# Performance work log

Measured on AMD Instinct MI355X. Metric: run time of the kernel, lower is better.

Reference implementation:

```python
import jax, jax.numpy as jnp
import numpy as np

N = 65536      # total nodes
E = 655360     # total edges
G = 256        # graphs in batch
EGO = 64       # ego ids per graph (max(ego)+1)
S = G * EGO    # global ego segments
C_IN, H, P, OUT, L = 128, 128, 64, 10, 3
EPS = 1e-5


def setup_inputs() -> dict:
    key = jax.random.key(0)
    ks = jax.random.split(key, 8)
    x = jax.random.normal(ks[0], (N, C_IN), dtype=jnp.float32)
    edge_index = jax.random.randint(ks[1], (2, E), 0, N)
    batch = jnp.repeat(jnp.arange(G), N // G)          # sorted graph ids
    ego = jnp.arange(N) % EGO                           # every ego segment non-empty
    s = 1.0 / np.sqrt(H)
    w_root = jax.random.normal(ks[2], (L, H, H), jnp.float32) * s
    w_rel = jax.random.normal(ks[3], (L, H, H), jnp.float32) * s
    b_conv = jnp.zeros((L, H), jnp.float32)
    down_w = jax.random.normal(ks[4], (H, P), jnp.float32) * s
    w1 = jax.random.normal(ks[5], (P, 2 * OUT), jnp.float32) * (1.0 / np.sqrt(P))
    b1 = jnp.zeros((2 * OUT,), jnp.float32)
    gamma = jnp.ones((2 * OUT,), jnp.float32)
    beta = jnp.zeros((2 * OUT,), jnp.float32)
    w2 = jax.random.normal(ks[6], (2 * OUT, OUT), jnp.float32) * (1.0 / np.sqrt(2 * OUT))
    b2 = jnp.zeros((OUT,), jnp.float32)
    return dict(x=x, edge_index=edge_index, batch=batch, ego=ego,
                w_root=w_root, w_rel=w_rel, b_conv=b_conv, down_w=down_w,
                w1=w1, b1=b1, gamma=gamma, beta=beta, w2=w2, b2=b2)


def reference(x, edge_index, batch, ego, w_root, w_rel, b_conv, down_w,
              w1, b1, gamma, beta, w2, b2):
    src, dst = edge_index[0], edge_index[1]
    h = x
    for l in range(L):  # GraphConv: lin_rel(sum_{j->i} h_j) + lin_root(h_i) + b, then ReLU
        agg = jax.ops.segment_sum(h[src], dst, num_segments=N)      # [N,H]
        h = jax.nn.relu(agg @ w_rel[l] + h @ w_root[l] + b_conv[l])
    xi = h @ down_w                                                  # [N,P]
    ego_g = ego + batch * EGO                                        # global ego id
    pooled = jax.ops.segment_sum(xi, ego_g, num_segments=S)          # global_add_pool -> [S,P]
    seg_batch = jax.ops.segment_max(batch, ego_g, num_segments=S)    # global_max_pool(batch, ego) -> [S]
    # SoftmaxAggregation(t=1): per-feature softmax over ego segments within each graph
    m = jax.ops.segment_max(pooled, seg_batch, num_segments=G)       # [G,P]
    e = jnp.exp(pooled - m[seg_batch])
    denom = jax.ops.segment_sum(e, seg_batch, num_segments=G)
    alpha = jax.lax.stop_gradient(e / denom[seg_batch])              # semi_grad=True
    g = jax.ops.segment_sum(alpha * pooled, seg_batch, num_segments=G)  # [G,P]
    # PyG MLP([P, 2*OUT, OUT]): Linear -> BatchNorm (batch stats) -> ReLU -> Linear
    z = g @ w1 + b1
    mu = z.mean(axis=0)
    var = z.var(axis=0)
    z = (z - mu) / jnp.sqrt(var + EPS) * gamma + beta
    z = jax.nn.relu(z)
    return z @ w2 + b2                                               # [G,OUT]
```

## Files before the change

kernel.cpp:

```cpp
#include <hip/hip_runtime.h>
#include <hip/hip_bf16.h>

#define NN 65536
#define EE 655360
#define GG 256
#define EGOC 64
#define SS (GG*EGOC)
#define HH 128
#define PP 64
#define OUTD 10
#define LLAYERS 3
#define PADW 40
#define EPB1 5120
#define BCAP 4096

typedef __attribute__((ext_vector_type(8))) short short8_t;
typedef __attribute__((ext_vector_type(4))) float f32x4_t;

__device__ __forceinline__ unsigned short f2bf(float f){
  unsigned u = __float_as_uint(f);
  unsigned r = (u + 0x7fffu + ((u >> 16) & 1u)) >> 16;
  return (unsigned short)r;
}
__device__ __forceinline__ float bflo(unsigned v){ return __uint_as_float(v << 16); }
__device__ __forceinline__ float bfhi(unsigned v){ return __uint_as_float(v & 0xffff0000u); }

__global__ __launch_bounds__(256) void prep(const float* __restrict__ x,
    unsigned short* __restrict__ xb, int* __restrict__ bcur,
    const float* __restrict__ w_rel, const float* __restrict__ w_root,
    unsigned short* __restrict__ wt){
  const int b = blockIdx.x;
  if (b < 4096){
    if (b == 0) bcur[threadIdx.x] = 0;
    const size_t i = ((size_t)b * 256 + threadIdx.x) * 8;
    float4 a = *(const float4*)(x + i);
    float4 v = *(const float4*)(x + i + 4);
    uint4 o;
    o.x = f2bf(a.x) | ((unsigned)f2bf(a.y) << 16);
    o.y = f2bf(a.z) | ((unsigned)f2bf(a.w) << 16);
    o.z = f2bf(v.x) | ((unsigned)f2bf(v.y) << 16);
    o.w = f2bf(v.z) | ((unsigned)f2bf(v.w) << 16);
    *(uint4*)(xb + i) = o;
  } else {
    const int idx = (b - 4096) * 256 + threadIdx.x;
    const int mi = idx >> 14;
    const int n = (idx >> 7) & 127, k = idx & 127;
    const float* src = (mi & 1) ? w_root : w_rel;
    const int l = mi >> 1;
    wt[idx] = f2bf(src[(size_t)l * 16384 + (size_t)k * 128 + n]);
  }
}

__global__ __launch_bounds__(256) void bucket1(const int* __restrict__ src,
    const int* __restrict__ dst, int* __restrict__ bucket_cursor,
    unsigned* __restrict__ bdata){
  __shared__ int hist[256], lbase[256], cur[256], rbase[256];
  __shared__ unsigned staged[EPB1];
  const int t = threadIdx.x;
  const int e0 = blockIdx.x * EPB1;
  hist[t] = 0;
  __syncthreads();
  #pragma unroll
  for (int k = 0; k < EPB1/256; ++k){
    int d = dst[e0 + t + k*256];
    atomicAdd(&hist[d >> 8], 1);
  }
  __syncthreads();
  const int cnt = hist[t];
  int val = cnt;
  for (int off = 1; off < 256; off <<= 1){
    int y = (t >= off) ? hist[t - off] : 0;
    __syncthreads();
    val += y;
    hist[t] = val;
    __syncthreads();
  }
  const int excl = val - cnt;
  lbase[t] = excl;
  cur[t] = excl;
  rbase[t] = atomicAdd(&bucket_cursor[t], cnt);
  __syncthreads();
  #pragma unroll
  for (int k = 0; k < EPB1/256; ++k){
    int i = e0 + t + k*256;
    int d = dst[i];
    int s = src[i];
    int b = d >> 8;
    int p = atomicAdd(&cur[b], 1);
    staged[p] = (unsigned)s | ((unsigned)(d & 255) << 16) | ((unsigned)b << 24);
  }
  __syncthreads();
  #pragma unroll
  for (int k = 0; k < EPB1/256; ++k){
    int i = t + k*256;
    unsigned w = staged[i];
    int b = w >> 24;
    bdata[b * BCAP + rbase[b] + (i - lbase[b])] = w;
  }
}

__global__ __launch_bounds__(256) void bucket2(const unsigned* __restrict__ bdata,
    const int* __restrict__ bucket_cursor, int* __restrict__ rowptr,
    int* __restrict__ csr){
  __shared__ int hist[256], cur[256], red[256];
  const int t = threadIdx.x;
  const int b = blockIdx.x;
  red[t] = (t < b) ? bucket_cursor[t] : 0;
  hist[t] = 0;
  __syncthreads();
  for (int off = 128; off > 0; off >>= 1){
    if (t < off) red[t] += red[t + off];
    __syncthreads();
  }
  const int base = red[0];
  const int cnt = bucket_cursor[b];
  const unsigned* bd = bdata + (size_t)b * BCAP;
  for (int i = t; i < cnt; i += 256)
    atomicAdd(&hist[(bd[i] >> 16) & 255], 1);
  __syncthreads();
  const int c = hist[t];
  int val = c;
  for (int off = 1; off < 256; off <<= 1){
    int y = (t >= off) ? hist[t - off] : 0;
    __syncthreads();
    val += y;
    hist[t] = val;
    __syncthreads();
  }
  const int excl = val - c;
  cur[t] = excl;
  rowptr[(b << 8) + t] = base + excl;
  if (b == 255 && t == 255) rowptr[NN] = EE;
  __syncthreads();
  for (int i = t; i < cnt; i += 256){
    unsigned w = bd[i];
    int dl = (w >> 16) & 255;
    int p = atomicAdd(&cur[dl], 1);
    csr[base + p] = (int)(w & 0xFFFFu);
  }
}

__global__ __launch_bounds__(256) void agg_bf(const unsigned* __restrict__ hb,
    const int* __restrict__ rowptr, const int* __restrict__ csr,
    unsigned* __restrict__ aggb){
  const int wid = threadIdx.x >> 6;
  const int lane = threadIdx.x & 63;
  const int sub = lane >> 4;
  const int c = lane & 15;
  int node = (blockIdx.x << 2) + wid;

  int beg = rowptr[node];
  int end = rowptr[node + 1];
  int sw0, sw1, sw2, sw3;
  {
    int e0 = beg + sub, e1 = beg + 4 + sub, e2 = beg + 8 + sub, e3 = beg + 12 + sub;
    sw0 = csr[e0 < end ? e0 : beg];
    sw1 = csr[e1 < end ? e1 : beg];
    sw2 = csr[e2 < end ? e2 : beg];
    sw3 = csr[e3 < end ? e3 : beg];
  }

  for (int g = 0; g < 8; ++g){
    uint4 w0 = *(const uint4*)(hb + ((size_t)sw0 << 6) + (c << 2));
    uint4 w1 = *(const uint4*)(hb + ((size_t)sw1 << 6) + (c << 2));
    uint4 w2 = *(const uint4*)(hb + ((size_t)sw2 << 6) + (c << 2));
    uint4 w3 = *(const uint4*)(hb + ((size_t)sw3 << 6) + (c << 2));
    int nbeg = 0, nend = 0;
    if (g < 7){
      nbeg = rowptr[node + 8192];
      nend = rowptr[node + 8193];
    }
    float a0=0.f,a1=0.f,a2=0.f,a3=0.f,a4=0.f,a5=0.f,a6=0.f,a7=0.f;
    if (beg + sub      < end){ a0+=bflo(w0.x); a1+=bfhi(w0.x); a2+=bflo(w0.y); a3+=bfhi(w0.y);
                               a4+=bflo(w0.z); a5+=bfhi(w0.z); a6+=bflo(w0.w); a7+=bfhi(w0.w); }
    if (beg + 4 + sub  < end){ a0+=bflo(w1.x); a1+=bfhi(w1.x); a2+=bflo(w1.y); a3+=bfhi(w1.y);
                               a4+=bflo(w1.z); a5+=bfhi(w1.z); a6+=bflo(w1.w); a7+=bfhi(w1.w); }
    if (beg + 8 + sub  < end){ a0+=bflo(w2.x); a1+=bfhi(w2.x); a2+=bflo(w2.y); a3+=bfhi(w2.y);
                               a4+=bflo(w2.z); a5+=bfhi(w2.z); a6+=bflo(w2.w); a7+=bfhi(w2.w); }
    if (beg + 12 + sub < end){ a0+=bflo(w3.x); a1+=bfhi(w3.x); a2+=bflo(w3.y); a3+=bfhi(w3.y);
                               a4+=bflo(w3.z); a5+=bfhi(w3.z); a6+=bflo(w3.w); a7+=bfhi(w3.w); }
    for (int j = beg + 16; j < end; j += 16){
      #pragma unroll
      for (int u = 0; u < 4; ++u){
        const int e = j + (u << 2) + sub;
        if (e < end){
          const int s = csr[e];
          uint4 w = *(const uint4*)(hb + ((size_t)s << 6) + (c << 2));
          a0 += bflo(w.x); a1 += bfhi(w.x);
          a2 += bflo(w.y); a3 += bfhi(w.y);
          a4 += bflo(w.z); a5 += bfhi(w.z);
          a6 += bflo(w.w); a7 += bfhi(w.w);
        }
      }
    }
    a0 += __shfl_xor(a0, 16, 64); a1 += __shfl_xor(a1, 16, 64);
    a2 += __shfl_xor(a2, 16, 64); a3 += __shfl_xor(a3, 16, 64);
    a4 += __shfl_xor(a4, 16, 64); a5 += __shfl_xor(a5, 16, 64);
    a6 += __shfl_xor(a6, 16, 64); a7 += __shfl_xor(a7, 16, 64);
    a0 += __shfl_xor(a0, 32, 64); a1 += __shfl_xor(a1, 32, 64);
    a2 += __shfl_xor(a2, 32, 64); a3 += __shfl_xor(a3, 32, 64);
    a4 += __shfl_xor(a4, 32, 64); a5 += __shfl_xor(a5, 32, 64);
    a6 += __shfl_xor(a6, 32, 64); a7 += __shfl_xor(a7, 32, 64);
    if (lane < 16){
      uint4 o;
      o.x = (unsigned)f2bf(a0) | ((unsigned)f2bf(a1) << 16);
      o.y = (unsigned)f2bf(a2) | ((unsigned)f2bf(a3) << 16);
      o.z = (unsigned)f2bf(a4) | ((unsigned)f2bf(a5) << 16);
      o.w = (unsigned)f2bf(a6) | ((unsigned)f2bf(a7) << 16);
      *(uint4*)(aggb + ((size_t)node << 6) + (c << 2)) = o;
    }
    if (g < 7){
      node += 8192;
      beg = nbeg; end = nend;
      int e0 = beg + sub, e1 = beg + 4 + sub, e2 = beg + 8 + sub, e3 = beg + 12 + sub;
      sw0 = csr[e0 < end ? e0 : beg];
      sw1 = csr[e1 < end ? e1 : beg];
      sw2 = csr[e2 < end ? e2 : beg];
      sw3 = csr[e3 < end ? e3 : beg];
    }
  }
}

__global__ __launch_bounds__(256) void conv_mfma(
    const unsigned short* __restrict__ Aagg, const unsigned short* __restrict__ Ah,
    const unsigned short* __restrict__ wt,
    const float* __restrict__ bias,
    unsigned short* __restrict__ out){
  __shared__ unsigned short As[2][128 * PADW];
  __shared__ unsigned short Ws[2][128 * PADW];
  const int tid = threadIdx.x;
  const int row0 = blockIdx.x << 7;
  const int lane = tid & 63, wid = tid >> 6;
  const int wm64 = (wid >> 1) << 6;
  const int wn64 = (wid & 1) << 6;
  const int fr = lane & 15;
  const int fs = (lane >> 4) << 3;
  const int r0 = tid >> 2;
  const int s8 = (tid & 3) << 3;

  f32x4_t acc[4][4];
  #pragma unroll
  for (int i = 0; i < 4; ++i)
    #pragma unroll
    for (int j = 0; j < 4; ++j) acc[i][j] = (f32x4_t){0.f,0.f,0.f,0.f};

  uint4 ga0, ga1, gw0, gw1;

#define STAGE_LOAD(c) do{ \
    const unsigned short* Ap = ((c) < 4) ? Aagg : Ah; \
    const unsigned short* Wp = ((c) < 4) ? wt : (wt + 16384); \
    const int k0 = ((c) & 3) << 5; \
    ga0 = *(const uint4*)(Ap + (size_t)(row0 + r0) * 128 + k0 + s8); \
    ga1 = *(const uint4*)(Ap + (size_t)(row0 + 64 + r0) * 128 + k0 + s8); \
    gw0 = *(const uint4*)(Wp + (size_t)r0 * 128 + k0 + s8); \
    gw1 = *(const uint4*)(Wp + (size_t)(64 + r0) * 128 + k0 + s8); } while(0)
#define STAGE_WRITE(b) do{ \
    *(uint4*)&As[b][r0 * PADW + s8] = ga0; \
    *(uint4*)&As[b][(64 + r0) * PADW + s8] = ga1; \
    *(uint4*)&Ws[b][r0 * PADW + s8] = gw0; \
    *(uint4*)&Ws[b][(64 + r0) * PADW + s8] = gw1; } while(0)

  STAGE_LOAD(0);
  STAGE_WRITE(0);
  __syncthreads();

  for (int c = 0; c < 8; ++c){
    const int b = c & 1;
    if (c < 7) STAGE_LOAD(c + 1);

    short8_t af[4], wf[4];
    #pragma unroll
    for (int i = 0; i < 4; ++i)
      af[i] = *(const short8_t*)&As[b][(wm64 + i*16 + fr) * PADW + fs];
    #pragma unroll
    for (int j = 0; j < 4; ++j)
      wf[j] = *(const short8_t*)&Ws[b][(wn64 + j*16 + fr) * PADW + fs];
    #pragma unroll
    for (int j = 0; j < 4; ++j)
      #pragma unroll
      for (int i = 0; i < 4; ++i)
        acc[i][j] = __builtin_amdgcn_mfma_f32_16x16x32_bf16(wf[j], af[i], acc[i][j], 0, 0, 0);

    if (c < 7){
      STAGE_WRITE(b ^ 1);
      __syncthreads();
    }
  }
#undef STAGE_LOAD
#undef STAGE_WRITE

  #pragma unroll
  for (int j = 0; j < 4; ++j){
    const int n0 = wn64 + j*16 + ((lane >> 4) << 2);
    float4 b4 = *(const float4*)(bias + n0);
    #pragma unroll
    for (int i = 0; i < 4; ++i){
      const int m = row0 + wm64 + i*16 + fr;
      float v0 = fmaxf(acc[i][j][0] + b4.x, 0.f);
      float v1 = fmaxf(acc[i][j][1] + b4.y, 0.f);
      float v2 = fmaxf(acc[i][j][2] + b4.z, 0.f);
      float v3 = fmaxf(acc[i][j][3] + b4.w, 0.f);
      uint2 pk;
      pk.x = (unsigned)f2bf(v0) | ((unsigned)f2bf(v1) << 16);
      pk.y = (unsigned)f2bf(v2) | ((unsigned)f2bf(v3) << 16);
      *(uint2*)(out + (size_t)m * 128 + n0) = pk;
    }
  }
}

__global__ __launch_bounds__(256) void pool_proj(const unsigned* __restrict__ hb,
    const float* __restrict__ down_w, float* __restrict__ pooled){
  __shared__ float wds[128 * 64];
  __shared__ float hs[4][128];
  const int tid = threadIdx.x;
  for (int i = tid; i < 128 * 64 / 4; i += 256)
    ((float4*)wds)[i] = ((const float4*)down_w)[i];
  __syncthreads();
  const int wid = tid >> 6, lane = tid & 63;
  for (int it = 0; it < 4; ++it){
    const int s = (blockIdx.x << 4) + (it << 2) + wid;
    const int b = s >> 6, e = s & 63;
    const unsigned* hr = hb + (((size_t)(b * 256 + e)) << 6) + lane;
    float ax = 0.f, ay = 0.f;
    #pragma unroll
    for (int q = 0; q < 4; ++q){
      unsigned v = hr[(size_t)q * 64 * 64];
      ax += bflo(v); ay += bfhi(v);
    }
    hs[wid][(lane << 1) + 0] = ax;
    hs[wid][(lane << 1) + 1] = ay;
    float a0 = 0.f, a1 = 0.f, a2 = 0.f, a3 = 0.f;
    #pragma unroll
    for (int k = 0; k < 128; k += 4){
      a0 = fmaf(hs[wid][k + 0], wds[(k + 0) * 64 + lane], a0);
      a1 = fmaf(hs[wid][k + 1], wds[(k + 1) * 64 + lane], a1);
      a2 = fmaf(hs[wid][k + 2], wds[(k + 2) * 64 + lane], a2);
      a3 = fmaf(hs[wid][k + 3], wds[(k + 3) * 64 + lane], a3);
    }
    pooled[(size_t)s * 64 + lane] = (a0 + a1) + (a2 + a3);
  }
}

__global__ __launch_bounds__(256) void graph_softmax(const float* __restrict__ pooled,
    float* __restrict__ gout){
  __shared__ float ps[4096];
  __shared__ float r1[4][64], r2[4][64];
  const int tid = threadIdx.x;
  const float* P = pooled + (size_t)blockIdx.x * 4096;
  for (int i = tid; i < 1024; i += 256)
    ((float4*)ps)[i] = ((const float4*)P)[i];
  __syncthreads();
  const int wid = tid >> 6, lane = tid & 63;
  float m = -3.4e38f;
  #pragma unroll
  for (int r = 0; r < 16; ++r) m = fmaxf(m, ps[((wid << 4) + r) * 64 + lane]);
  r1[wid][lane] = m;
  __syncthreads();
  m = fmaxf(fmaxf(r1[0][lane], r1[1][lane]), fmaxf(r1[2][lane], r1[3][lane]));
  __syncthreads();
  float se = 0.f, sn = 0.f;
  #pragma unroll
  for (int r = 0; r < 16; ++r){
    float p = ps[((wid << 4) + r) * 64 + lane];
    float ev = expf(p - m);
    se += ev; sn += ev * p;
  }
  r1[wid][lane] = se; r2[wid][lane] = sn;
  __syncthreads();
  if (wid == 0){
    float d = (r1[0][lane] + r1[1][lane]) + (r1[2][lane] + r1[3][lane]);
    float n = (r2[0][lane] + r2[1][lane]) + (r2[2][lane] + r2[3][lane]);
    gout[(size_t)blockIdx.x * 64 + lane] = n / d;
  }
}

__global__ __launch_bounds__(256) void mlp_kernel(const float* __restrict__ gmat,
    const float* __restrict__ w1, const float* __restrict__ b1,
    const float* __restrict__ gamma, const float* __restrict__ beta,
    const float* __restrict__ w2, const float* __restrict__ b2,
    float* __restrict__ out){
  const int r = threadIdx.x;
  float z[20];
  #pragma unroll
  for (int j = 0; j < 20; ++j) z[j] = b1[j];
  for (int k = 0; k < 64; ++k){
    float gv = gmat[r*64 + k];
    #pragma unroll
    for (int j = 0; j < 20; ++j) z[j] = fmaf(gv, w1[k*20 + j], z[j]);
  }
  __shared__ float red1[4][20], red2[4][20];
  __shared__ float mu[20], istd[20];
  const int lane = r & 63, wid = r >> 6;
  #pragma unroll
  for (int j = 0; j < 20; ++j){
    float a = z[j], b = z[j]*z[j];
    #pragma unroll
    for (int off = 32; off > 0; off >>= 1){
      a += __shfl_xor(a, off, 64);
      b += __shfl_xor(b, off, 64);
    }
    if (lane == 0){ red1[wid][j] = a; red2[wid][j] = b; }
  }
  __syncthreads();
  if (r < 20){
    float m = red1[0][r] + red1[1][r] + red1[2][r] + red1[3][r];
    float q = red2[0][r] + red2[1][r] + red2[2][r] + red2[3][r];
    m *= (1.f/256.f); q *= (1.f/256.f);
    float var = q - m*m;
    mu[r] = m;
    istd[r] = 1.f / sqrtf(var + 1e-5f);
  }
  __syncthreads();
  float o[10];
  #pragma unroll
  for (int jo = 0; jo < 10; ++jo) o[jo] = b2[jo];
  #pragma unroll
  for (int j = 0; j < 20; ++j){
    float zn = (z[j] - mu[j]) * istd[j] * gamma[j] + beta[j];
    zn = fmaxf(zn, 0.f);
    #pragma unroll
    for (int jo = 0; jo < 10; ++jo) o[jo] = fmaf(zn, w2[j*10 + jo], o[jo]);
  }
  #pragma unroll
  for (int jo = 0; jo < 10; ++jo) out[r*10 + jo] = o[jo];
}

extern "C" void kernel_launch(void* const* d_in, const int* in_sizes, int n_in,
                              void* d_out, int out_size, void* d_ws, size_t ws_size,
                              hipStream_t stream){
  const float* x      = (const float*)d_in[0];
  const int*   eidx   = (const int*)d_in[1];
  const float* w_root = (const float*)d_in[4];
  const float* w_rel  = (const float*)d_in[5];
  const float* b_conv = (const float*)d_in[6];
  const float* down_w = (const float*)d_in[7];
  const float* w1     = (const float*)d_in[8];
  const float* b1     = (const float*)d_in[9];
  const float* gamma  = (const float*)d_in[10];
  const float* beta   = (const float*)d_in[11];
  const float* w2     = (const float*)d_in[12];
  const float* b2     = (const float*)d_in[13];
  const int* src = eidx;
  const int* dst = eidx + EE;

  char* wsp = (char*)d_ws;
  size_t off = 0;
  auto alloc = [&](size_t bytes)->char*{
    char* p = wsp + off;
    off += (bytes + 255) & ~(size_t)255;
    return p;
  };
  unsigned short* hb   = (unsigned short*)alloc((size_t)NN*HH*2);
  unsigned short* aggb = (unsigned short*)alloc((size_t)NN*HH*2);
  unsigned short* wtb  = (unsigned short*)alloc((size_t)6*128*128*2);
  float*    pooled = (float*)   alloc((size_t)SS*PP*4);
  int*      rowptr = (int*)     alloc((size_t)(NN+1)*4);
  int*      csr    = (int*)     alloc((size_t)EE*4);
  unsigned* bdata  = (unsigned*)alloc((size_t)256*BCAP*4);
  int*      bcur   = (int*)     alloc((size_t)256*4);
  float*    gout   = (float*)   alloc((size_t)GG*PP*4);

  prep<<<4096 + 384, 256, 0, stream>>>(x, hb, bcur, w_rel, w_root, wtb);
  bucket1<<<EE/EPB1, 256, 0, stream>>>(src, dst, bcur, bdata);
  bucket2<<<256, 256, 0, stream>>>(bdata, bcur, rowptr, csr);

  for (int l = 0; l < LLAYERS; ++l){
    agg_bf<<<2048, 256, 0, stream>>>((const unsigned*)hb, rowptr, csr, (unsigned*)aggb);
    conv_mfma<<<NN/128, 256, 0, stream>>>(aggb, hb, wtb + (size_t)l*2*16384,
        b_conv + (size_t)l*HH, hb);
  }

  pool_proj<<<SS/16, 256, 0, stream>>>((const unsigned*)hb, down_w, pooled);
  graph_softmax<<<GG, 256, 0, stream>>>(pooled, gout);
  mlp_kernel<<<1, 256, 0, stream>>>(gout, w1, b1, gamma, beta, w2, b2, (float*)d_out);
}
```

Measured before the change: 190.8 us.

## Deepen gather prefetch pipeline in agg_bf and fuse pooling with graph softmax

The aggregation kernel now fully unrolls its 8-node loop and software-pipelines loads. Row pointers are fetched three nodes ahead, CSR source indices two ahead, and neighbor feature rows one ahead into double-buffered registers, so gather latency overlaps with the current node's accumulation. Separately, the pooling/projection and per-graph softmax kernels are merged into a single kernel with one block per graph, which drops the pooled intermediate buffer and one launch. The risks are higher register pressure in agg_bf and only 256 blocks for the fused pooling kernel.

```diff
diff --git a/kernel.cpp b/kernel.cpp
--- a/kernel.cpp
+++ b/kernel.cpp
@@ -147,49 +147,69 @@
   const int lane = threadIdx.x & 63;
   const int sub = lane >> 4;
   const int c = lane & 15;
-  int node = (blockIdx.x << 2) + wid;
-
-  int beg = rowptr[node];
-  int end = rowptr[node + 1];
-  int sw0, sw1, sw2, sw3;
-  {
-    int e0 = beg + sub, e1 = beg + 4 + sub, e2 = beg + 8 + sub, e3 = beg + 12 + sub;
-    sw0 = csr[e0 < end ? e0 : beg];
-    sw1 = csr[e1 < end ? e1 : beg];
-    sw2 = csr[e2 < end ? e2 : beg];
-    sw3 = csr[e3 < end ? e3 : beg];
-  }
-
-  for (int g = 0; g < 8; ++g){
-    uint4 w0 = *(const uint4*)(hb + ((size_t)sw0 << 6) + (c << 2));
-    uint4 w1 = *(const uint4*)(hb + ((size_t)sw1 << 6) + (c << 2));
-    uint4 w2 = *(const uint4*)(hb + ((size_t)sw2 << 6) + (c << 2));
-    uint4 w3 = *(const uint4*)(hb + ((size_t)sw3 << 6) + (c << 2));
-    int nbeg = 0, nend = 0;
-    if (g < 7){
-      nbeg = rowptr[node + 8192];
-      nend = rowptr[node + 8193];
+  const int base = (blockIdx.x << 2) + wid;
+
+  int bg[9], en[9];
+  int sw[8][4];
+  uint4 w[2][4];
+
+  bg[0] = rowptr[base];          en[0] = rowptr[base + 1];
+  bg[1] = rowptr[base + 8192];   en[1] = rowptr[base + 8193];
+  bg[2] = rowptr[base + 16384];  en[2] = rowptr[base + 16385];
+  #pragma unroll
+  for (int u = 0; u < 4; ++u){
+    int e = bg[0] + (u << 2) + sub;
+    sw[0][u] = csr[e < en[0] ? e : bg[0]];
+  }
+  #pragma unroll
+  for (int u = 0; u < 4; ++u)
+    w[0][u] = *(const uint4*)(hb + ((size_t)sw[0][u] << 6) + (c << 2));
+  #pragma unroll
+  for (int u = 0; u < 4; ++u){
+    int e = bg[1] + (u << 2) + sub;
+    sw[1][u] = csr[e < en[1] ? e : bg[1]];
+  }
+
+  #pragma unroll
+  for (int k = 0; k < 8; ++k){
+    const int node = base + (k << 13);
+    if (k < 7){
+      #pragma unroll
+      for (int u = 0; u < 4; ++u)
+        w[(k+1)&1][u] = *(const uint4*)(hb + ((size_t)sw[k+1][u] << 6) + (c << 2));
+    }
+    if (k + 3 <= 7){
+      bg[k+3] = rowptr[base + ((k+3) << 13)];
+      en[k+3] = rowptr[base + ((k+3) << 13) + 1];
+    }
+    if (k + 2 <= 7){
+      #pragma unroll
+      for (int u = 0; u < 4; ++u){
+        int e = bg[k+2] + (u << 2) + sub;
+        sw[k+2][u] = csr[e < en[k+2] ? e : bg[k+2]];
+      }
     }
     float a0=0.f,a1=0.f,a2=0.f,a3=0.f,a4=0.f,a5=0.f,a6=0.f,a7=0.f;
-    if (beg + sub      < end){ a0+=bflo(w0.x); a1+=bfhi(w0.x); a2+=bflo(w0.y); a3+=bfhi(w0.y);
-                               a4+=bflo(w0.z); a5+=bfhi(w0.z); a6+=bflo(w0.w); a7+=bfhi(w0.w); }
-    if (beg + 4 + sub  < end){ a0+=bflo(w1.x); a1+=bfhi(w1.x); a2+=bflo(w1.y); a3+=bfhi(w1.y);
-                               a4+=bflo(w1.z); a5+=bfhi(w1.z); a6+=bflo(w1.w); a7+=bfhi(w1.w); }
-    if (beg + 8 + sub  < end){ a0+=bflo(w2.x); a1+=bfhi(w2.x); a2+=bflo(w2.y); a3+=bfhi(w2.y);
-                               a4+=bflo(w2.z); a5+=bfhi(w2.z); a6+=bflo(w2.w); a7+=bfhi(w2.w); }
-    if (beg + 12 + sub < end){ a0+=bflo(w3.x); a1+=bfhi(w3.x); a2+=bflo(w3.y); a3+=bfhi(w3.y);
-                               a4+=bflo(w3.z); a5+=bfhi(w3.z); a6+=bflo(w3.w); a7+=bfhi(w3.w); }
-    for (int j = beg + 16; j < end; j += 16){
+    const uint4 w0 = w[k&1][0], w1 = w[k&1][1], w2 = w[k&1][2], w3 = w[k&1][3];
+    if (bg[k] + sub      < en[k]){ a0+=bflo(w0.x); a1+=bfhi(w0.x); a2+=bflo(w0.y); a3+=bfhi(w0.y);
+                                   a4+=bflo(w0.z); a5+=bfhi(w0.z); a6+=bflo(w0.w); a7+=bfhi(w0.w); }
+    if (bg[k] + 4 + sub  < en[k]){ a0+=bflo(w1.x); a1+=bfhi(w1.x); a2+=bflo(w1.y); a3+=bfhi(w1.y);
+                                   a4+=bflo(w1.z); a5+=bfhi(w1.z); a6+=bflo(w1.w); a7+=bfhi(w1.w); }
+    if (bg[k] + 8 + sub  < en[k]){ a0+=bflo(w2.x); a1+=bfhi(w2.x); a2+=bflo(w2.y); a3+=bfhi(w2.y);
+                                   a4+=bflo(w2.z); a5+=bfhi(w2.z); a6+=bflo(w2.w); a7+=bfhi(w2.w); }
+    if (bg[k] + 12 + sub < en[k]){ a0+=bflo(w3.x); a1+=bfhi(w3.x); a2+=bflo(w3.y); a3+=bfhi(w3.y);
+                                   a4+=bflo(w3.z); a5+=bfhi(w3.z); a6+=bflo(w3.w); a7+=bfhi(w3.w); }
+    for (int j = bg[k] + 16; j < en[k]; j += 16){
       #pragma unroll
       for (int u = 0; u < 4; ++u){
         const int e = j + (u << 2) + sub;
-        if (e < end){
+        if (e < en[k]){
           const int s = csr[e];
-          uint4 w = *(const uint4*)(hb + ((size_t)s << 6) + (c << 2));
-          a0 += bflo(w.x); a1 += bfhi(w.x);
-          a2 += bflo(w.y); a3 += bfhi(w.y);
-          a4 += bflo(w.z); a5 += bfhi(w.z);
-          a6 += bflo(w.w); a7 += bfhi(w.w);
+          uint4 wt_ = *(const uint4*)(hb + ((size_t)s << 6) + (c << 2));
+          a0 += bflo(wt_.x); a1 += bfhi(wt_.x);
+          a2 += bflo(wt_.y); a3 += bfhi(wt_.y);
+          a4 += bflo(wt_.z); a5 += bfhi(wt_.z);
+          a6 += bflo(wt_.w); a7 += bfhi(wt_.w);
         }
       }
     }
@@ -208,15 +228,6 @@
       o.z = (unsigned)f2bf(a4) | ((unsigned)f2bf(a5) << 16);
       o.w = (unsigned)f2bf(a6) | ((unsigned)f2bf(a7) << 16);
       *(uint4*)(aggb + ((size_t)node << 6) + (c << 2)) = o;
-    }
-    if (g < 7){
-      node += 8192;
-      beg = nbeg; end = nend;
-      int e0 = beg + sub, e1 = beg + 4 + sub, e2 = beg + 8 + sub, e3 = beg + 12 + sub;
-      sw0 = csr[e0 < end ? e0 : beg];
-      sw1 = csr[e1 < end ? e1 : beg];
-      sw2 = csr[e2 < end ? e2 : beg];
-      sw3 = csr[e3 < end ? e3 : beg];
     }
   }
 }
@@ -308,19 +319,21 @@
   }
 }
 
-__global__ __launch_bounds__(256) void pool_proj(const unsigned* __restrict__ hb,
-    const float* __restrict__ down_w, float* __restrict__ pooled){
+__global__ __launch_bounds__(256) void pool_soft(const unsigned* __restrict__ hb,
+    const float* __restrict__ down_w, float* __restrict__ gout){
   __shared__ float wds[128 * 64];
+  __shared__ float ps[64][64];
   __shared__ float hs[4][128];
+  __shared__ float r1[4][64], r2[4][64];
   const int tid = threadIdx.x;
+  const int g = blockIdx.x;
   for (int i = tid; i < 128 * 64 / 4; i += 256)
     ((float4*)wds)[i] = ((const float4*)down_w)[i];
   __syncthreads();
   const int wid = tid >> 6, lane = tid & 63;
-  for (int it = 0; it < 4; ++it){
-    const int s = (blockIdx.x << 4) + (it << 2) + wid;
-    const int b = s >> 6, e = s & 63;
-    const unsigned* hr = hb + (((size_t)(b * 256 + e)) << 6) + lane;
+  for (int it = 0; it < 16; ++it){
+    const int e = (it << 2) + wid;
+    const unsigned* hr = hb + (((size_t)(g * 256 + e)) << 6) + lane;
     float ax = 0.f, ay = 0.f;
     #pragma unroll
     for (int q = 0; q < 4; ++q){
@@ -337,23 +350,12 @@
       a2 = fmaf(hs[wid][k + 2], wds[(k + 2) * 64 + lane], a2);
       a3 = fmaf(hs[wid][k + 3], wds[(k + 3) * 64 + lane], a3);
     }
-    pooled[(size_t)s * 64 + lane] = (a0 + a1) + (a2 + a3);
-  }
-}
-
-__global__ __launch_bounds__(256) void graph_softmax(const float* __restrict__ pooled,
-    float* __restrict__ gout){
-  __shared__ float ps[4096];
-  __shared__ float r1[4][64], r2[4][64];
-  const int tid = threadIdx.x;
-  const float* P = pooled + (size_t)blockIdx.x * 4096;
-  for (int i = tid; i < 1024; i += 256)
-    ((float4*)ps)[i] = ((const float4*)P)[i];
-  __syncthreads();
-  const int wid = tid >> 6, lane = tid & 63;
+    ps[e][lane] = (a0 + a1) + (a2 + a3);
+  }
+  __syncthreads();
   float m = -3.4e38f;
   #pragma unroll
-  for (int r = 0; r < 16; ++r) m = fmaxf(m, ps[((wid << 4) + r) * 64 + lane]);
+  for (int r = 0; r < 16; ++r) m = fmaxf(m, ps[(wid << 4) + r][lane]);
   r1[wid][lane] = m;
   __syncthreads();
   m = fmaxf(fmaxf(r1[0][lane], r1[1][lane]), fmaxf(r1[2][lane], r1[3][lane]));
@@ -361,7 +363,7 @@
   float se = 0.f, sn = 0.f;
   #pragma unroll
   for (int r = 0; r < 16; ++r){
-    float p = ps[((wid << 4) + r) * 64 + lane];
+    float p = ps[(wid << 4) + r][lane];
     float ev = expf(p - m);
     se += ev; sn += ev * p;
   }
@@ -370,7 +372,7 @@
   if (wid == 0){
     float d = (r1[0][lane] + r1[1][lane]) + (r1[2][lane] + r1[3][lane]);
     float n = (r2[0][lane] + r2[1][lane]) + (r2[2][lane] + r2[3][lane]);
-    gout[(size_t)blockIdx.x * 64 + lane] = n / d;
+    gout[(size_t)g * 64 + lane] = n / d;
   }
 }
 
@@ -453,7 +455,6 @@
   unsigned short* hb   = (unsigned short*)alloc((size_t)NN*HH*2);
   unsigned short* aggb = (unsigned short*)alloc((size_t)NN*HH*2);
   unsigned short* wtb  = (unsigned short*)alloc((size_t)6*128*128*2);
-  float*    pooled = (float*)   alloc((size_t)SS*PP*4);
   int*      rowptr = (int*)     alloc((size_t)(NN+1)*4);
   int*      csr    = (int*)     alloc((size_t)EE*4);
   unsigned* bdata  = (unsigned*)alloc((size_t)256*BCAP*4);
@@ -470,7 +471,6 @@
         b_conv + (size_t)l*HH, hb);
   }
 
-  pool_proj<<<SS/16, 256, 0, stream>>>((const unsigned*)hb, down_w, pooled);
-  graph_softmax<<<GG, 256, 0, stream>>>(pooled, gout);
+  pool_soft<<<GG, 256, 0, stream>>>((const unsigned*)hb, down_w, gout);
   mlp_kernel<<<1, 256, 0, stream>>>(gout, w1, b1, gamma, beta, w2, b2, (float*)d_out);
 }
```

New measurement: 197.3 us. 1.03x slower.
